# Optimization experiments

Hardware: AMD Instinct MI355X
Metric: run time of the kernel (lower is better)

## Reference

```python
import jax, jax.numpy as jnp
import numpy as np

N, T, V, CIN, COUT = 64, 12, 256, 64, 64


def _conv1x1(h, w, b):
    # h: [n,c,v,w], w: [o,c] (1x1 conv kernel squeezed), b: [o]
    return jnp.einsum('ncvw,oc->novw', h, w) + b[None, :, None, None]


def setup_inputs() -> dict:
    key = jax.random.key(0)
    ks = jax.random.split(key, 8)
    x = jax.random.normal(ks[0], (N, CIN, T, V), jnp.float32)
    feats = jax.random.normal(ks[1], (N, 7, V, V), jnp.float32)
    mask = (jax.random.uniform(ks[2], (N, 1, V, V)) < 0.3).astype(jnp.float32)
    A = jnp.concatenate([feats, mask], axis=1)  # [N, 8, V, V]
    init = lambda k, shape, fan: jax.random.normal(k, shape, jnp.float32) / np.sqrt(fan).astype(np.float32)
    conv_w = init(ks[3], (COUT, CIN), CIN)
    conv_b = jnp.zeros((COUT,), jnp.float32)
    w1 = init(ks[4], (16, 7), 7)
    b1 = jnp.zeros((16,), jnp.float32)
    w2 = init(ks[5], (32, 16), 16)
    b2 = jnp.zeros((32,), jnp.float32)
    w3 = init(ks[6], (64, 32), 32)
    b3 = jnp.zeros((64,), jnp.float32)
    return dict(x=x, A=A, conv_w=conv_w, conv_b=conv_b,
                w1=w1, b1=b1, w2=w2, b2=b2, w3=w3, b3=b3)


def reference(x, A, conv_w, conv_b, w1, b1, w2, b2, w3, b3):
    # 1x1 temporal conv on node features: [n,cin,t,v] -> [n,cout,t,v]
    x = jnp.einsum('nctv,oc->notv', x, conv_w) + conv_b[None, :, None, None]
    mask = A[:, 7:]          # [n,1,v,v]
    h = A[:, :7]             # [n,7,v,v]
    # adjmatder MLP (dropout is identity at inference)
    h = jax.nn.relu(_conv1x1(h, w1, b1))
    h = jax.nn.relu(_conv1x1(h, w2, b2))
    h = jax.nn.relu(_conv1x1(h, w3, b3))   # [n,64,v,v]
    Aw = h * mask
    # per-channel graph convolution: [n,c,t,v] x [n,c,v,w] -> [n,c,t,w]
    out = jnp.einsum('nctv,ncvw->nctw', x, Aw)
    return out, Aw
```

## Files before the change

kernel.cpp:

```cpp
#include <hip/hip_runtime.h>
#include <hip/hip_bf16.h>

#define NB   64
#define TT   12
#define VV   256
#define CIN  64
#define COUT 64
#define VSQ  65536
#define PP   256

typedef float f32x4 __attribute__((ext_vector_type(4)));

__global__ __launch_bounds__(256) void k1_conv(
    const float* __restrict__ x, const float* __restrict__ w,
    const float* __restrict__ b, float* __restrict__ y)
{
    const int nt = blockIdx.x;
    const int n  = nt / TT;
    const int t  = nt % TT;
    const int v  = threadIdx.x;

    const float* xp = x + ((long)n * CIN * TT + t) * VV + v;
    float xv[CIN];
    #pragma unroll 8
    for (int c = 0; c < CIN; ++c)
        xv[c] = xp[(long)c * TT * VV];

    float* yp = y + ((long)n * COUT * TT + t) * VV + v;

    for (int o0 = 0; o0 < COUT; o0 += 16) {
        float acc[16];
        #pragma unroll
        for (int i = 0; i < 16; ++i) acc[i] = b[o0 + i];
        #pragma unroll 8
        for (int c = 0; c < CIN; ++c) {
            const float xc = xv[c];
            #pragma unroll
            for (int i = 0; i < 16; ++i)
                acc[i] += w[(o0 + i) * CIN + c] * xc;
        }
        #pragma unroll
        for (int i = 0; i < 16; ++i)
            yp[(long)(o0 + i) * TT * VV] = acc[i];
    }
}

__global__ __launch_bounds__(256) void k2_mlp(
    const float* __restrict__ A,
    const float* __restrict__ w1, const float* __restrict__ b1,
    const float* __restrict__ w2, const float* __restrict__ b2,
    const float* __restrict__ w3, const float* __restrict__ b3,
    float* __restrict__ Aw)
{
    __shared__ float h2s[32][260];
    __shared__ float ms[PP];

    const int  tid  = threadIdx.x;
    const long gpos = (long)blockIdx.x * PP;
    const int  n    = (int)(gpos >> 16);
    const int  rem0 = (int)(gpos & (VSQ - 1));

    {
        const float* ap = A + ((long)n * 8 << 16) + rem0 + tid;
        float f[7];
        #pragma unroll
        for (int c = 0; c < 7; ++c) f[c] = ap[(long)c << 16];
        ms[tid] = ap[(long)7 << 16];

        float h1[16];
        #pragma unroll
        for (int o = 0; o < 16; ++o) {
            float s = b1[o];
            #pragma unroll
            for (int k = 0; k < 7; ++k) s += w1[o * 7 + k] * f[k];
            h1[o] = fmaxf(s, 0.f);
        }
        #pragma unroll
        for (int o = 0; o < 32; ++o) {
            float s = b2[o];
            #pragma unroll
            for (int k = 0; k < 16; ++k) s += w2[o * 16 + k] * h1[k];
            h2s[o][tid] = fmaxf(s, 0.f);
        }
    }
    __syncthreads();

    const int cq = tid >> 4;
    const int pl = tid & 15;

    float w3r[4][32];
    #pragma unroll
    for (int i = 0; i < 4; ++i) {
        #pragma unroll
        for (int k4 = 0; k4 < 32; k4 += 4) {
            const f32x4 wv = *reinterpret_cast<const f32x4*>(&w3[(cq * 4 + i) * 32 + k4]);
            w3r[i][k4 + 0] = wv.x; w3r[i][k4 + 1] = wv.y;
            w3r[i][k4 + 2] = wv.z; w3r[i][k4 + 3] = wv.w;
        }
    }
    const float bb0 = b3[cq * 4 + 0], bb1 = b3[cq * 4 + 1];
    const float bb2 = b3[cq * 4 + 2], bb3 = b3[cq * 4 + 3];

    float* awbase = Aw + ((long)n * COUT << 16) + rem0;

    #pragma unroll
    for (int iter = 0; iter < 4; ++iter) {
        const int q = pl + iter * 16;
        f32x4 a0 = (f32x4)(bb0), a1 = (f32x4)(bb1);
        f32x4 a2 = (f32x4)(bb2), a3 = (f32x4)(bb3);
        #pragma unroll
        for (int k = 0; k < 32; ++k) {
            const f32x4 h = *reinterpret_cast<const f32x4*>(&h2s[k][q * 4]);
            a0 += w3r[0][k] * h;
            a1 += w3r[1][k] * h;
            a2 += w3r[2][k] * h;
            a3 += w3r[3][k] * h;
        }
        const f32x4 m4 = *reinterpret_cast<const f32x4*>(&ms[q * 4]);
        f32x4 r0, r1, r2, r3;
        #pragma unroll
        for (int j = 0; j < 4; ++j) {
            r0[j] = fmaxf(a0[j], 0.f) * m4[j];
            r1[j] = fmaxf(a1[j], 0.f) * m4[j];
            r2[j] = fmaxf(a2[j], 0.f) * m4[j];
            r3[j] = fmaxf(a3[j], 0.f) * m4[j];
        }
        const int pq = q * 4;
        __builtin_nontemporal_store(r0, reinterpret_cast<f32x4*>(awbase + ((long)(cq * 4 + 0) << 16) + pq));
        __builtin_nontemporal_store(r1, reinterpret_cast<f32x4*>(awbase + ((long)(cq * 4 + 1) << 16) + pq));
        __builtin_nontemporal_store(r2, reinterpret_cast<f32x4*>(awbase + ((long)(cq * 4 + 2) << 16) + pq));
        __builtin_nontemporal_store(r3, reinterpret_cast<f32x4*>(awbase + ((long)(cq * 4 + 3) << 16) + pq));
    }
}

__global__ __launch_bounds__(256) void k3_einsum(
    const float* __restrict__ Aw, const float* __restrict__ y,
    float* __restrict__ out)
{
    __shared__ float ys[4][TT][VV];

    const int n   = blockIdx.x >> 4;
    const int c0  = (blockIdx.x & 15) * 4;
    const int tid = threadIdx.x;
    const int cq  = tid >> 6;
    const int w4  = (tid & 63) * 4;

    {
        const float* src = y + ((long)(n * COUT + c0) * TT) * VV;
        float* dst = &ys[0][0][0];
        #pragma unroll
        for (int it = 0; it < 12; ++it) {
            const int idx = tid + it * 256;
            *reinterpret_cast<float4*>(dst + idx * 4) =
                *reinterpret_cast<const float4*>(src + idx * 4);
        }
    }
    __syncthreads();

    const float* awp = Aw + (((long)(n * COUT + c0 + cq)) << 16) + w4;
    float4 acc[TT];
    #pragma unroll
    for (int t = 0; t < TT; ++t) acc[t] = make_float4(0.f, 0.f, 0.f, 0.f);

    for (int v0 = 0; v0 < VV; v0 += 4) {
        float4 xs[TT];
        #pragma unroll
        for (int t = 0; t < TT; ++t)
            xs[t] = *reinterpret_cast<const float4*>(&ys[cq][t][v0]);

        const f32x4 aw0 = __builtin_nontemporal_load(
            reinterpret_cast<const f32x4*>(awp + (long)(v0 + 0) * VV));
        const f32x4 aw1 = __builtin_nontemporal_load(
            reinterpret_cast<const f32x4*>(awp + (long)(v0 + 1) * VV));
        const f32x4 aw2 = __builtin_nontemporal_load(
            reinterpret_cast<const f32x4*>(awp + (long)(v0 + 2) * VV));
        const f32x4 aw3 = __builtin_nontemporal_load(
            reinterpret_cast<const f32x4*>(awp + (long)(v0 + 3) * VV));

        #pragma unroll
        for (int t = 0; t < TT; ++t) {
            acc[t].x += xs[t].x * aw0.x + xs[t].y * aw1.x + xs[t].z * aw2.x + xs[t].w * aw3.x;
            acc[t].y += xs[t].x * aw0.y + xs[t].y * aw1.y + xs[t].z * aw2.y + xs[t].w * aw3.y;
            acc[t].z += xs[t].x * aw0.z + xs[t].y * aw1.z + xs[t].z * aw2.z + xs[t].w * aw3.z;
            acc[t].w += xs[t].x * aw0.w + xs[t].y * aw1.w + xs[t].z * aw2.w + xs[t].w * aw3.w;
        }
    }

    float* op = out + ((long)(n * COUT + c0 + cq) * TT) * VV + w4;
    #pragma unroll
    for (int t = 0; t < TT; ++t)
        *reinterpret_cast<float4*>(op + t * VV) = acc[t];
}

extern "C" void kernel_launch(void* const* d_in, const int* in_sizes, int n_in,
                              void* d_out, int out_size, void* d_ws, size_t ws_size,
                              hipStream_t stream)
{
    const float* x      = (const float*)d_in[0];
    const float* A      = (const float*)d_in[1];
    const float* conv_w = (const float*)d_in[2];
    const float* conv_b = (const float*)d_in[3];
    const float* w1     = (const float*)d_in[4];
    const float* b1     = (const float*)d_in[5];
    const float* w2     = (const float*)d_in[6];
    const float* b2     = (const float*)d_in[7];
    const float* w3     = (const float*)d_in[8];
    const float* b3     = (const float*)d_in[9];

    float* out = (float*)d_out;
    float* Aw  = (float*)d_out + (long)NB * COUT * TT * VV;
    const size_t y_bytes = (size_t)NB * COUT * TT * VV * sizeof(float);

    float* y = (ws_size >= y_bytes) ? (float*)d_ws : out;

    k1_conv<<<NB * TT, 256, 0, stream>>>(x, conv_w, conv_b, y);

    k2_mlp<<<(NB * VSQ) / PP, 256, 0, stream>>>(A, w1, b1, w2, b2, w3, b3, Aw);

    k3_einsum<<<NB * (COUT / 4), 256, 0, stream>>>(Aw, y, out);
}
```

Measured before the change: 668.1 us.

## Compute third MLP layer with bf16 MFMA instead of FP32 FMA

The 32->64 third MLP layer in k2_mlp now runs on 16x16x32 bf16 MFMA instructions. h2 activations are packed into bf16 pairs in a fragment layout in shared memory, and w3 is converted to bf16 B fragments per lane. The aim is to cut the FP32 FMA and LDS traffic of that layer. In exchange, the layer loses precision through bf16 rounding, and the output store pattern changes to per-lane 16-byte stores strided across channels.

New measurement: 638.8 us. 4.4% less time.

```diff
diff --git a/kernel.cpp b/kernel.cpp
--- a/kernel.cpp
+++ b/kernel.cpp
@@ -7,9 +7,15 @@
 #define CIN  64
 #define COUT 64
 #define VSQ  65536
-#define PP   256
 
 typedef float f32x4 __attribute__((ext_vector_type(4)));
+using s16x8 = __attribute__((ext_vector_type(8))) short;
+
+__device__ __forceinline__ unsigned short f2bf(float f) {
+    union { __hip_bfloat16 h; unsigned short u; } cv;
+    cv.h = __float2bfloat16(f);
+    return cv.u;
+}
 
 __global__ __launch_bounds__(256) void k1_conv(
     const float* __restrict__ x, const float* __restrict__ w,
@@ -52,11 +58,11 @@
     const float* __restrict__ w3, const float* __restrict__ b3,
     float* __restrict__ Aw)
 {
-    __shared__ float h2s[32][260];
-    __shared__ float ms[PP];
+    __shared__ unsigned int afrag[16 * 256];
+    __shared__ float ms[256];
 
     const int  tid  = threadIdx.x;
-    const long gpos = (long)blockIdx.x * PP;
+    const long gpos = (long)blockIdx.x * 256;
     const int  n    = (int)(gpos >> 16);
     const int  rem0 = (int)(gpos & (VSQ - 1));
 
@@ -75,61 +81,62 @@
             for (int k = 0; k < 7; ++k) s += w1[o * 7 + k] * f[k];
             h1[o] = fmaxf(s, 0.f);
         }
+        float h2[32];
         #pragma unroll
         for (int o = 0; o < 32; ++o) {
             float s = b2[o];
             #pragma unroll
             for (int k = 0; k < 16; ++k) s += w2[o * 16 + k] * h1[k];
-            h2s[o][tid] = fmaxf(s, 0.f);
+            h2[o] = fmaxf(s, 0.f);
+        }
+
+        const int m = tid >> 4;
+        const int r = tid & 15;
+        #pragma unroll
+        for (int kk = 0; kk < 16; ++kk) {
+            const unsigned int pr = (unsigned int)f2bf(h2[2 * kk])
+                                  | ((unsigned int)f2bf(h2[2 * kk + 1]) << 16);
+            afrag[m * 256 + (kk >> 2) * 64 + r * 4 + (kk & 3)] = pr;
         }
     }
     __syncthreads();
 
-    const int cq = tid >> 4;
-    const int pl = tid & 15;
-
-    float w3r[4][32];
-    #pragma unroll
-    for (int i = 0; i < 4; ++i) {
-        #pragma unroll
-        for (int k4 = 0; k4 < 32; k4 += 4) {
-            const f32x4 wv = *reinterpret_cast<const f32x4*>(&w3[(cq * 4 + i) * 32 + k4]);
-            w3r[i][k4 + 0] = wv.x; w3r[i][k4 + 1] = wv.y;
-            w3r[i][k4 + 2] = wv.z; w3r[i][k4 + 3] = wv.w;
-        }
-    }
-    const float bb0 = b3[cq * 4 + 0], bb1 = b3[cq * 4 + 1];
-    const float bb2 = b3[cq * 4 + 2], bb3 = b3[cq * 4 + 3];
+    const int lane = tid & 63;
+    const int wave = tid >> 6;
+    const int lc   = lane & 15;
+    const int lq   = lane >> 4;
+
+    s16x8 bfr[4];
+    float bias[4];
+    #pragma unroll
+    for (int ntile = 0; ntile < 4; ++ntile) {
+        const int c = ntile * 16 + lc;
+        const float* wr = w3 + c * 32 + lq * 8;
+        s16x8 bf;
+        #pragma unroll
+        for (int i = 0; i < 8; ++i) bf[i] = (short)f2bf(wr[i]);
+        bfr[ntile]  = bf;
+        bias[ntile] = b3[c];
+    }
 
     float* awbase = Aw + ((long)n * COUT << 16) + rem0;
 
     #pragma unroll
-    for (int iter = 0; iter < 4; ++iter) {
-        const int q = pl + iter * 16;
-        f32x4 a0 = (f32x4)(bb0), a1 = (f32x4)(bb1);
-        f32x4 a2 = (f32x4)(bb2), a3 = (f32x4)(bb3);
-        #pragma unroll
-        for (int k = 0; k < 32; ++k) {
-            const f32x4 h = *reinterpret_cast<const f32x4*>(&h2s[k][q * 4]);
-            a0 += w3r[0][k] * h;
-            a1 += w3r[1][k] * h;
-            a2 += w3r[2][k] * h;
-            a3 += w3r[3][k] * h;
-        }
-        const f32x4 m4 = *reinterpret_cast<const f32x4*>(&ms[q * 4]);
-        f32x4 r0, r1, r2, r3;
-        #pragma unroll
-        for (int j = 0; j < 4; ++j) {
-            r0[j] = fmaxf(a0[j], 0.f) * m4[j];
-            r1[j] = fmaxf(a1[j], 0.f) * m4[j];
-            r2[j] = fmaxf(a2[j], 0.f) * m4[j];
-            r3[j] = fmaxf(a3[j], 0.f) * m4[j];
-        }
-        const int pq = q * 4;
-        __builtin_nontemporal_store(r0, reinterpret_cast<f32x4*>(awbase + ((long)(cq * 4 + 0) << 16) + pq));
-        __builtin_nontemporal_store(r1, reinterpret_cast<f32x4*>(awbase + ((long)(cq * 4 + 1) << 16) + pq));
-        __builtin_nontemporal_store(r2, reinterpret_cast<f32x4*>(awbase + ((long)(cq * 4 + 2) << 16) + pq));
-        __builtin_nontemporal_store(r3, reinterpret_cast<f32x4*>(awbase + ((long)(cq * 4 + 3) << 16) + pq));
+    for (int j = 0; j < 4; ++j) {
+        const int mt = wave * 4 + j;
+        const s16x8 afr = *reinterpret_cast<const s16x8*>(&afrag[mt * 256 + lane * 4]);
+        const int pbase = mt * 16 + lq * 4;
+        const f32x4 mv = *reinterpret_cast<const f32x4*>(&ms[pbase]);
+        #pragma unroll
+        for (int ntile = 0; ntile < 4; ++ntile) {
+            f32x4 acc = (f32x4)(bias[ntile]);
+            acc = __builtin_amdgcn_mfma_f32_16x16x32_bf16(afr, bfr[ntile], acc, 0, 0, 0);
+            f32x4 r;
+            #pragma unroll
+            for (int u = 0; u < 4; ++u) r[u] = fmaxf(acc[u], 0.f) * mv[u];
+            __builtin_nontemporal_store(r, reinterpret_cast<f32x4*>(
+                awbase + ((long)(ntile * 16 + lc) << 16) + pbase));
+        }
     }
 }
 
@@ -215,7 +222,7 @@
 
     k1_conv<<<NB * TT, 256, 0, stream>>>(x, conv_w, conv_b, y);
 
-    k2_mlp<<<(NB * VSQ) / PP, 256, 0, stream>>>(A, w1, b1, w2, b2, w3, b3, Aw);
+    k2_mlp<<<(NB * VSQ) / 256, 256, 0, stream>>>(A, w1, b1, w2, b2, w3, b3, Aw);
 
     k3_einsum<<<NB * (COUT / 4), 256, 0, stream>>>(Aw, y, out);
 }
```
